# Performance work log

Hardware: AMD Instinct MI355X
Metric: run time of the kernel (lower is better)

The kernel has to match this reference:

```python
import jax, jax.numpy as jnp
import numpy as np

N = 50000      # nodes
E = 600000     # edges
D_IN = 5
D_H = 128
EPS = 1e-5     # BatchNorm1d default eps


def batch_norm(x, gamma, beta):
    # training-mode BN over the node dimension (biased variance)
    m = jnp.mean(x, axis=0)
    v = jnp.var(x, axis=0)
    return (x - m) * jax.lax.rsqrt(v + EPS) * gamma + beta


def gcn_conv(x, W, b, src, dst, w):
    # PyG GCNConv: linear transform, add self-loops (weight 1),
    # symmetric normalization D^-1/2 A D^-1/2, scatter-add to dst, + bias.
    x = x @ W                                   # [N, out]
    n = x.shape[0]
    loop = jnp.arange(n)
    src = jnp.concatenate([src, loop])
    dst = jnp.concatenate([dst, loop])
    w = jnp.concatenate([w, jnp.ones((n,), w.dtype)])
    deg = jax.ops.segment_sum(w, dst, num_segments=n)
    dis = jnp.where(deg > 0, jax.lax.rsqrt(jnp.maximum(deg, 1e-12)), 0.0)
    norm = dis[src] * w * dis[dst]              # [E+N]
    msgs = norm[:, None] * x[src]               # gather + scale
    return jax.ops.segment_sum(msgs, dst, num_segments=n) + b


def setup_inputs() -> dict:
    key = jax.random.key(0)
    ks = jax.random.split(key, 20)
    s_in = 1.0 / np.sqrt(D_IN)
    s_h = 1.0 / np.sqrt(D_H)
    return {
        "h": jax.random.normal(ks[0], (N, D_IN), jnp.float32),
        "edge_index": jax.random.randint(ks[1], (2, E), 0, N),
        "edge_weight": jax.random.uniform(ks[2], (E,), jnp.float32),
        "g0": 1.0 + 0.1 * jax.random.normal(ks[3], (D_IN,), jnp.float32),
        "be0": 0.1 * jax.random.normal(ks[4], (D_IN,), jnp.float32),
        "W1": jax.random.normal(ks[5], (D_IN, D_H), jnp.float32) * s_in,
        "b1": jax.random.normal(ks[6], (D_H,), jnp.float32) * s_in,
        "g1": 1.0 + 0.1 * jax.random.normal(ks[7], (D_H,), jnp.float32),
        "be1": 0.1 * jax.random.normal(ks[8], (D_H,), jnp.float32),
        "W2": jax.random.normal(ks[9], (D_H, D_H), jnp.float32) * s_h,
        "b2": jax.random.normal(ks[10], (D_H,), jnp.float32) * s_h,
        "g2": 1.0 + 0.1 * jax.random.normal(ks[11], (D_H,), jnp.float32),
        "be2": 0.1 * jax.random.normal(ks[12], (D_H,), jnp.float32),
        "Wmu": jax.random.normal(ks[13], (D_H, D_H), jnp.float32) * s_h,
        "bmu": jax.random.normal(ks[14], (D_H,), jnp.float32) * s_h,
        "Wls": jax.random.normal(ks[15], (D_H, D_H), jnp.float32) * s_h,
        "bls": jax.random.normal(ks[16], (D_H,), jnp.float32) * s_h,
    }


def reference(h, edge_index, edge_weight, g0, be0, W1, b1, g1, be1,
              W2, b2, g2, be2, Wmu, bmu, Wls, bls):
    src, dst = edge_index[0], edge_index[1]
    h = batch_norm(h, g0, be0)
    h = jax.nn.relu(batch_norm(gcn_conv(h, W1, b1, src, dst, edge_weight), g1, be1))
    # dropout p=0.1 treated as eval-mode (identity)
    h = jax.nn.relu(batch_norm(gcn_conv(h, W2, b2, src, dst, edge_weight), g2, be2))
    mu = h @ Wmu + bmu
    log_std = h @ Wls + bls
    return (mu, log_std)
```

## Files before the change

kernel.cpp:

```cpp
#include <hip/hip_runtime.h>

#define N_NODES 50000
#define N_EDGES 600000
#define D_IN 5
#define D_H 128
#define BN_EPS 1e-5f
#define SCAN_BLOCKS ((N_NODES + 255) / 256)
#define DEG_BLOCKS ((N_EDGES + 255) / 256)
#define FIX_SCALE 16777216.0f
#define FIX_INV   (1.0f / 16777216.0f)

typedef __bf16 bf16x8 __attribute__((ext_vector_type(8)));
typedef float  f32x4  __attribute__((ext_vector_type(4)));

__device__ inline unsigned short f2bfb(float f) {
    unsigned u = __builtin_bit_cast(unsigned, f);
    unsigned r = u + 0x7fffu + ((u >> 16) & 1u);
    return (unsigned short)(r >> 16);
}
__device__ inline float bflo(unsigned u) { return __builtin_bit_cast(float, u << 16); }
__device__ inline float bfhi(unsigned u) { return __builtin_bit_cast(float, u & 0xffff0000u); }

__device__ inline void stage_b(const unsigned short* __restrict__ Bt,
                               uint4* __restrict__ lds, int t)
{
#pragma unroll
    for (int i = 0; i < 8; ++i) {
        int slot = i * 256 + t;
        int fid = slot >> 6;
        int l = slot & 63;
        int row = (fid >> 2) * 16 + (l & 15);
        int boff = ((l >> 4) * 16 + (fid & 3) * 64) >> 1;
        lds[slot] = *(const uint4*)(Bt + row * D_H + boff);
    }
}

__global__ __launch_bounds__(256) void k_prep(const float* __restrict__ W2,
                                              const float* __restrict__ Wmu,
                                              const float* __restrict__ Wls,
                                              unsigned short* __restrict__ T2,
                                              unsigned short* __restrict__ Tmu,
                                              unsigned short* __restrict__ Tls,
                                              const float* __restrict__ h,
                                              float* __restrict__ stats0,
                                              const int* __restrict__ dst,
                                              const float* __restrict__ w,
                                              unsigned long long* __restrict__ degcnt,
                                              int* __restrict__ rank)
{
    __shared__ float ss[D_IN], sq[D_IN];
    int b = blockIdx.x;
    int t = threadIdx.x;
    if (b < 192) {
        int mat = b >> 6;
        int idx = (b & 63) * 256 + t;
        const float* W = (mat == 0) ? W2 : (mat == 1) ? Wmu : Wls;
        unsigned short* T = (mat == 0) ? T2 : (mat == 1) ? Tmu : Tls;
        int k = idx >> 7, n = idx & 127;
        T[n * D_H + k] = f2bfb(W[idx]);
    } else if (b < 192 + SCAN_BLOCKS) {
        if (t < D_IN) { ss[t] = 0.f; sq[t] = 0.f; }
        __syncthreads();
        int node = (b - 192) * 256 + t;
        float v[D_IN];
#pragma unroll
        for (int f = 0; f < D_IN; ++f)
            v[f] = (node < N_NODES) ? h[node * D_IN + f] : 0.f;
        int lane = t & 63;
#pragma unroll
        for (int f = 0; f < D_IN; ++f) {
            float s = v[f], q = v[f] * v[f];
            for (int off = 32; off > 0; off >>= 1) {
                s += __shfl_down(s, off);
                q += __shfl_down(q, off);
            }
            if (lane == 0) { atomicAdd(&ss[f], s); atomicAdd(&sq[f], q); }
        }
        __syncthreads();
        if (t < D_IN) {
            atomicAdd(&stats0[t], ss[t]);
            atomicAdd(&stats0[D_IN + t], sq[t]);
        }
    } else {
        int e = (b - 192 - SCAN_BLOCKS) * 256 + t;
        if (e < N_EDGES) {
            int d = dst[e];
            unsigned long long fx = (unsigned long long)(w[e] * FIX_SCALE + 0.5f);
            unsigned long long old = atomicAdd(degcnt + d, (1ull << 40) | fx);
            rank[e] = (int)(old >> 40);
        }
    }
}

__global__ __launch_bounds__(256) void k_scan1(const unsigned long long* __restrict__ degcnt,
                                               float* __restrict__ dis,
                                               int* __restrict__ blocksums)
{
    __shared__ int sm[256];
    int t = threadIdx.x;
    int i = blockIdx.x * 256 + t;
    int c = 0;
    if (i < N_NODES) {
        unsigned long long v = degcnt[i];
        c = (int)(v >> 40);
        float deg = (float)(v & ((1ull << 40) - 1)) * FIX_INV;
        dis[i] = rsqrtf(deg + 1.0f);
    }
    sm[t] = c;
    __syncthreads();
    for (int off = 128; off > 0; off >>= 1) {
        if (t < off) sm[t] += sm[t + off];
        __syncthreads();
    }
    if (t == 0) blocksums[blockIdx.x] = sm[0];
}

__global__ __launch_bounds__(256) void k_scan2(int* __restrict__ blocksums,
                                               int* __restrict__ rowptr)
{
    __shared__ int sm[256];
    int t = threadIdx.x;
    int c = (t < SCAN_BLOCKS) ? blocksums[t] : 0;
    sm[t] = c;
    __syncthreads();
    for (int off = 1; off < 256; off <<= 1) {
        int v = (t >= off) ? sm[t - off] : 0;
        __syncthreads();
        sm[t] += v;
        __syncthreads();
    }
    if (t < SCAN_BLOCKS) blocksums[t] = sm[t] - c;
    if (t == 255) rowptr[N_NODES] = sm[255];
}

__global__ __launch_bounds__(256) void k_scan3(const unsigned long long* __restrict__ degcnt,
                                               int* __restrict__ rowptr,
                                               const int* __restrict__ blocksums)
{
    __shared__ int sm[256];
    int t = threadIdx.x;
    int i = blockIdx.x * 256 + t;
    int c = (i < N_NODES) ? (int)(degcnt[i] >> 40) : 0;
    sm[t] = c;
    __syncthreads();
    for (int off = 1; off < 256; off <<= 1) {
        int v = (t >= off) ? sm[t - off] : 0;
        __syncthreads();
        sm[t] += v;
        __syncthreads();
    }
    if (i < N_NODES)
        rowptr[i] = blocksums[blockIdx.x] + sm[t] - c;
}

__global__ __launch_bounds__(256) void k_fill(const int* __restrict__ src,
                                              const int* __restrict__ dst,
                                              const float* __restrict__ w,
                                              const float* __restrict__ dis,
                                              const int* __restrict__ rowptr,
                                              const int* __restrict__ rank,
                                              int2* __restrict__ csr)
{
    int e = blockIdx.x * blockDim.x + threadIdx.x;
    if (e < N_EDGES) {
        int s = src[e], d = dst[e];
        float pn = dis[s] * w[e];
        int pos = rowptr[d] + rank[e];
        int2 pk;
        pk.x = s;
        pk.y = __builtin_bit_cast(int, pn);
        csr[pos] = pk;
    }
}

__global__ __launch_bounds__(256) void k_agg0(const float* __restrict__ h,
                                              const float* __restrict__ stats,
                                              const float* __restrict__ g0,
                                              const float* __restrict__ be0,
                                              const int* __restrict__ rowptr,
                                              const int2* __restrict__ csr,
                                              const float* __restrict__ dis,
                                              float* __restrict__ agg)
{
    int n = blockIdx.x * blockDim.x + threadIdx.x;
    if (n >= N_NODES) return;
    float sc[D_IN], sh[D_IN];
#pragma unroll
    for (int f = 0; f < D_IN; ++f) {
        float m = stats[f] * (1.0f / N_NODES);
        float var = stats[D_IN + f] * (1.0f / N_NODES) - m * m;
        sc[f] = rsqrtf(var + BN_EPS) * g0[f];
        sh[f] = be0[f] - m * sc[f];
    }
    float dn = dis[n];
    float acc[D_IN];
#pragma unroll
    for (int f = 0; f < D_IN; ++f)
        acc[f] = dn * (h[n * D_IN + f] * sc[f] + sh[f]);
    int e0 = rowptr[n], e1 = rowptr[n + 1];
    for (int e = e0; e < e1; ++e) {
        int2 pk = csr[e];
        int s = pk.x;
        float pn = __builtin_bit_cast(float, pk.y);
#pragma unroll
        for (int f = 0; f < D_IN; ++f)
            acc[f] += pn * (h[s * D_IN + f] * sc[f] + sh[f]);
    }
#pragma unroll
    for (int f = 0; f < D_IN; ++f)
        agg[n * D_IN + f] = dn * acc[f];
}

__global__ __launch_bounds__(256) void k_l1(const float* __restrict__ agg,
                                            const float* __restrict__ W1,
                                            const float* __restrict__ b1,
                                            unsigned short* __restrict__ x,
                                            float* __restrict__ stats)
{
    __shared__ float sm_s[D_H], sm_q[D_H];
    int t = threadIdx.x;
    if (t < D_H) { sm_s[t] = 0.f; sm_q[t] = 0.f; }
    __syncthreads();
    int idx0 = blockIdx.x * 256 + t;
    int f0 = (idx0 & 63) * 2;
    float wa[D_IN], wb[D_IN];
#pragma unroll
    for (int k = 0; k < D_IN; ++k) {
        wa[k] = W1[k * D_H + f0];
        wb[k] = W1[k * D_H + f0 + 1];
    }
    float ba = b1[f0], bb = b1[f0 + 1];
    float s0 = 0.f, q0 = 0.f, s1 = 0.f, q1 = 0.f;
    const int stride = 512 * 256;
    for (int idx = idx0; idx < N_NODES * 64; idx += stride) {
        int n = idx >> 6;
        const float* a = agg + n * D_IN;
        float v0 = ba, v1 = bb;
#pragma unroll
        for (int k = 0; k < D_IN; ++k) { v0 += wa[k] * a[k]; v1 += wb[k] * a[k]; }
        ((unsigned*)x)[idx] = (unsigned)f2bfb(v0) | ((unsigned)f2bfb(v1) << 16);
        s0 += v0; q0 += v0 * v0; s1 += v1; q1 += v1 * v1;
    }
    atomicAdd(&sm_s[f0], s0); atomicAdd(&sm_s[f0 + 1], s1);
    atomicAdd(&sm_q[f0], q0); atomicAdd(&sm_q[f0 + 1], q1);
    __syncthreads();
    if (t < D_H) {
        atomicAdd(stats + t, sm_s[t]);
        atomicAdd(stats + D_H + t, sm_q[t]);
    }
}

__global__ __launch_bounds__(256) void k_agg128(const unsigned short* __restrict__ x,
                                                const float* __restrict__ stats,
                                                const float* __restrict__ g,
                                                const float* __restrict__ be,
                                                const int* __restrict__ rowptr,
                                                const int2* __restrict__ csr,
                                                const float* __restrict__ dis,
                                                unsigned short* __restrict__ outb)
{
    int t = threadIdx.x;
    int n = blockIdx.x * 16 + (t >> 4);
    int f0 = (t & 15) * 8;
    if (n >= N_NODES) return;
    float sc[8], sh[8];
    const float inv = 1.0f / N_NODES;
#pragma unroll
    for (int j = 0; j < 8; ++j) {
        float m = stats[f0 + j] * inv;
        float var = stats[D_H + f0 + j] * inv - m * m;
        sc[j] = rsqrtf(var + BN_EPS) * g[f0 + j];
        sh[j] = be[f0 + j] - m * sc[j];
    }
#define BNR(val, j) fmaxf((val) * sc[j] + sh[j], 0.f)
    float dn = dis[n];
    uint4 hv = *(const uint4*)(x + (size_t)n * D_H + f0);
    float a0 = dn * BNR(bflo(hv.x), 0), a1 = dn * BNR(bfhi(hv.x), 1);
    float a2 = dn * BNR(bflo(hv.y), 2), a3 = dn * BNR(bfhi(hv.y), 3);
    float a4 = dn * BNR(bflo(hv.z), 4), a5 = dn * BNR(bfhi(hv.z), 5);
    float a6 = dn * BNR(bflo(hv.w), 6), a7 = dn * BNR(bfhi(hv.w), 7);
    int e = rowptr[n], e1 = rowptr[n + 1];
    for (; e + 4 <= e1; e += 4) {
        int2 p0 = csr[e + 0], p1 = csr[e + 1], p2 = csr[e + 2], p3 = csr[e + 3];
        float w0 = __builtin_bit_cast(float, p0.y);
        float w1 = __builtin_bit_cast(float, p1.y);
        float w2 = __builtin_bit_cast(float, p2.y);
        float w3 = __builtin_bit_cast(float, p3.y);
        uint4 v0 = *(const uint4*)(x + (size_t)p0.x * D_H + f0);
        uint4 v1 = *(const uint4*)(x + (size_t)p1.x * D_H + f0);
        uint4 v2 = *(const uint4*)(x + (size_t)p2.x * D_H + f0);
        uint4 v3 = *(const uint4*)(x + (size_t)p3.x * D_H + f0);
        a0 += w0 * BNR(bflo(v0.x), 0) + w1 * BNR(bflo(v1.x), 0) + w2 * BNR(bflo(v2.x), 0) + w3 * BNR(bflo(v3.x), 0);
        a1 += w0 * BNR(bfhi(v0.x), 1) + w1 * BNR(bfhi(v1.x), 1) + w2 * BNR(bfhi(v2.x), 1) + w3 * BNR(bfhi(v3.x), 1);
        a2 += w0 * BNR(bflo(v0.y), 2) + w1 * BNR(bflo(v1.y), 2) + w2 * BNR(bflo(v2.y), 2) + w3 * BNR(bflo(v3.y), 2);
        a3 += w0 * BNR(bfhi(v0.y), 3) + w1 * BNR(bfhi(v1.y), 3) + w2 * BNR(bfhi(v2.y), 3) + w3 * BNR(bfhi(v3.y), 3);
        a4 += w0 * BNR(bflo(v0.z), 4) + w1 * BNR(bflo(v1.z), 4) + w2 * BNR(bflo(v2.z), 4) + w3 * BNR(bflo(v3.z), 4);
        a5 += w0 * BNR(bfhi(v0.z), 5) + w1 * BNR(bfhi(v1.z), 5) + w2 * BNR(bfhi(v2.z), 5) + w3 * BNR(bfhi(v3.z), 5);
        a6 += w0 * BNR(bflo(v0.w), 6) + w1 * BNR(bflo(v1.w), 6) + w2 * BNR(bflo(v2.w), 6) + w3 * BNR(bflo(v3.w), 6);
        a7 += w0 * BNR(bfhi(v0.w), 7) + w1 * BNR(bfhi(v1.w), 7) + w2 * BNR(bfhi(v2.w), 7) + w3 * BNR(bfhi(v3.w), 7);
    }
    for (; e < e1; ++e) {
        int2 pk = csr[e];
        float pn = __builtin_bit_cast(float, pk.y);
        uint4 v = *(const uint4*)(x + (size_t)pk.x * D_H + f0);
        a0 += pn * BNR(bflo(v.x), 0); a1 += pn * BNR(bfhi(v.x), 1);
        a2 += pn * BNR(bflo(v.y), 2); a3 += pn * BNR(bfhi(v.y), 3);
        a4 += pn * BNR(bflo(v.z), 4); a5 += pn * BNR(bfhi(v.z), 5);
        a6 += pn * BNR(bflo(v.w), 6); a7 += pn * BNR(bfhi(v.w), 7);
    }
#undef BNR
    uint4 o;
    o.x = (unsigned)f2bfb(dn * a0) | ((unsigned)f2bfb(dn * a1) << 16);
    o.y = (unsigned)f2bfb(dn * a2) | ((unsigned)f2bfb(dn * a3) << 16);
    o.z = (unsigned)f2bfb(dn * a4) | ((unsigned)f2bfb(dn * a5) << 16);
    o.w = (unsigned)f2bfb(dn * a6) | ((unsigned)f2bfb(dn * a7) << 16);
    *(uint4*)(outb + (size_t)n * D_H + f0) = o;
}

__global__ __launch_bounds__(256) void k_gemm_mf(const unsigned short* __restrict__ A,
                                                 const unsigned short* __restrict__ Bt,
                                                 const float* __restrict__ bias,
                                                 unsigned short* __restrict__ C,
                                                 float* __restrict__ stats)
{
    __shared__ uint4 ldsB[2048];
    __shared__ float sm_s[D_H], sm_q[D_H];
    int t = threadIdx.x;
    if (t < D_H) { sm_s[t] = 0.f; sm_q[t] = 0.f; }
    stage_b(Bt, ldsB, t);
    int wave = t >> 6, lane = t & 63;
    int m = lane & 15, quad = lane >> 4;
    int r0 = blockIdx.x * 64 + wave * 16;
    int arow = r0 + m < N_NODES ? r0 + m : N_NODES - 1;
    const bf16x8* ap = (const bf16x8*)(A + (size_t)arow * D_H + quad * 8);
    bf16x8 af[4];
#pragma unroll
    for (int ks = 0; ks < 4; ++ks) af[ks] = ap[ks * 4];
    __syncthreads();
    const bf16x8* bf = (const bf16x8*)ldsB;
    f32x4 acc[8];
#pragma unroll
    for (int ct = 0; ct < 8; ++ct) acc[ct] = (f32x4)(0.f);
#pragma unroll
    for (int ks = 0; ks < 4; ++ks) {
#pragma unroll
        for (int ct = 0; ct < 8; ++ct) {
            acc[ct] = __builtin_amdgcn_mfma_f32_16x16x32_bf16(
                af[ks], bf[(ct * 4 + ks) * 64 + lane], acc[ct], 0, 0, 0);
        }
    }
#pragma unroll
    for (int ct = 0; ct < 8; ++ct) {
        int col = ct * 16 + m;
        float bv = bias[col];
        float s = 0.f, q = 0.f;
#pragma unroll
        for (int r = 0; r < 4; ++r) {
            int rr = r0 + quad * 4 + r;
            if (rr < N_NODES) {
                float v = acc[ct][r] + bv;
                C[(size_t)rr * D_H + col] = f2bfb(v);
                s += v; q += v * v;
            }
        }
        atomicAdd(&sm_s[col], s);
        atomicAdd(&sm_q[col], q);
    }
    __syncthreads();
    if (t < D_H) {
        atomicAdd(stats + t, sm_s[t]);
        atomicAdd(stats + D_H + t, sm_q[t]);
    }
}

__global__ __launch_bounds__(256) void k_gemm_out_mf(const unsigned short* __restrict__ A,
                                                     const float* __restrict__ stats,
                                                     const float* __restrict__ g,
                                                     const float* __restrict__ be,
                                                     const unsigned short* __restrict__ Btmu,
                                                     const float* __restrict__ bmu,
                                                     const unsigned short* __restrict__ Btls,
                                                     const float* __restrict__ bls,
                                                     float* __restrict__ out)
{
    __shared__ uint4 ldsB[2048];
    int t = threadIdx.x;
    int wave = t >> 6, lane = t & 63;
    int m = lane & 15, quad = lane >> 4;
    int r0 = blockIdx.x * 64 + wave * 16;
    int arow = r0 + m < N_NODES ? r0 + m : N_NODES - 1;
    const unsigned short* arowp = A + (size_t)arow * D_H + quad * 8;
    const float inv = 1.0f / N_NODES;
    bf16x8 af[4];
#pragma unroll
    for (int ks = 0; ks < 4; ++ks) {
        uint4 av = *(const uint4*)(arowp + ks * 32);
        float vals[8] = { bflo(av.x), bfhi(av.x), bflo(av.y), bfhi(av.y),
                          bflo(av.z), bfhi(av.z), bflo(av.w), bfhi(av.w) };
        int fb = quad * 8 + ks * 32;
        unsigned short o[8];
#pragma unroll
        for (int j = 0; j < 8; ++j) {
            int f = fb + j;
            float mm = stats[f] * inv;
            float var = stats[D_H + f] * inv - mm * mm;
            float scv = rsqrtf(var + BN_EPS) * g[f];
            float shv = be[f] - mm * scv;
            o[j] = f2bfb(fmaxf(vals[j] * scv + shv, 0.f));
        }
        uint4 pk;
        pk.x = (unsigned)o[0] | ((unsigned)o[1] << 16);
        pk.y = (unsigned)o[2] | ((unsigned)o[3] << 16);
        pk.z = (unsigned)o[4] | ((unsigned)o[5] << 16);
        pk.w = (unsigned)o[6] | ((unsigned)o[7] << 16);
        af[ks] = __builtin_bit_cast(bf16x8, pk);
    }
    const bf16x8* bf = (const bf16x8*)ldsB;
#pragma unroll
    for (int half = 0; half < 2; ++half) {
        if (half) __syncthreads();
        stage_b(half ? Btls : Btmu, ldsB, t);
        __syncthreads();
        const float* bias = half ? bls : bmu;
        float* C = out + (half ? (size_t)N_NODES * D_H : 0);
        f32x4 acc[8];
#pragma unroll
        for (int ct = 0; ct < 8; ++ct) acc[ct] = (f32x4)(0.f);
#pragma unroll
        for (int ks = 0; ks < 4; ++ks) {
#pragma unroll
            for (int ct = 0; ct < 8; ++ct) {
                acc[ct] = __builtin_amdgcn_mfma_f32_16x16x32_bf16(
                    af[ks], bf[(ct * 4 + ks) * 64 + lane], acc[ct], 0, 0, 0);
            }
        }
#pragma unroll
        for (int ct = 0; ct < 8; ++ct) {
            int col = ct * 16 + m;
            float bv = bias[col];
#pragma unroll
            for (int r = 0; r < 4; ++r) {
                int rr = r0 + quad * 4 + r;
                if (rr < N_NODES)
                    C[(size_t)rr * D_H + col] = acc[ct][r] + bv;
            }
        }
    }
}

extern "C" void kernel_launch(void* const* d_in, const int* in_sizes, int n_in,
                              void* d_out, int out_size, void* d_ws, size_t ws_size,
                              hipStream_t stream)
{
    const float* h   = (const float*)d_in[0];
    const int*   eidx = (const int*)d_in[1];
    const float* ew  = (const float*)d_in[2];
    const float* g0  = (const float*)d_in[3];
    const float* be0 = (const float*)d_in[4];
    const float* W1  = (const float*)d_in[5];
    const float* b1  = (const float*)d_in[6];
    const float* g1  = (const float*)d_in[7];
    const float* be1 = (const float*)d_in[8];
    const float* W2  = (const float*)d_in[9];
    const float* b2  = (const float*)d_in[10];
    const float* g2  = (const float*)d_in[11];
    const float* be2 = (const float*)d_in[12];
    const float* Wmu = (const float*)d_in[13];
    const float* bmu = (const float*)d_in[14];
    const float* Wls = (const float*)d_in[15];
    const float* bls = (const float*)d_in[16];
    const int* srcv = eidx;
    const int* dstv = eidx + N_EDGES;
    float* out = (float*)d_out;

    char* ws = (char*)d_ws;
    size_t off = 0;
    auto alloc = [&](size_t bytes) -> char* {
        char* p = ws + off;
        off += (bytes + 255) & ~(size_t)255;
        return p;
    };
    float* stats0  = (float*)alloc(16 * 4);
    float* stats1  = (float*)alloc(256 * 4);
    float* stats2  = (float*)alloc(256 * 4);
    unsigned long long* degcnt = (unsigned long long*)alloc(N_NODES * 8);
    size_t zero_bytes = off;
    int*   rowptr  = (int*)  alloc((N_NODES + 1) * 4);
    float* dis     = (float*)alloc(N_NODES * 4);
    int*   rank    = (int*)  alloc((size_t)N_EDGES * 4);
    int*   blocksums = (int*)alloc(256 * 4);
    int2*  csr     = (int2*) alloc((size_t)N_EDGES * 8);
    float* agg0    = (float*)alloc(N_NODES * D_IN * 4);
    unsigned short* x1h  = (unsigned short*)alloc((size_t)N_NODES * D_H * 2);
    unsigned short* aggh = (unsigned short*)alloc((size_t)N_NODES * D_H * 2);
    unsigned short* c2h  = (unsigned short*)alloc((size_t)N_NODES * D_H * 2);
    unsigned short* Wt2   = (unsigned short*)alloc(D_H * D_H * 2);
    unsigned short* Wtmu  = (unsigned short*)alloc(D_H * D_H * 2);
    unsigned short* Wtls  = (unsigned short*)alloc(D_H * D_H * 2);
    (void)ws_size; (void)in_sizes; (void)n_in; (void)out_size;

    hipMemsetAsync(d_ws, 0, zero_bytes, stream);

    k_prep<<<192 + SCAN_BLOCKS + DEG_BLOCKS, 256, 0, stream>>>(
        W2, Wmu, Wls, Wt2, Wtmu, Wtls, h, stats0, dstv, ew, degcnt, rank);
    k_scan1<<<SCAN_BLOCKS, 256, 0, stream>>>(degcnt, dis, blocksums);
    k_scan2<<<1, 256, 0, stream>>>(blocksums, rowptr);
    k_scan3<<<SCAN_BLOCKS, 256, 0, stream>>>(degcnt, rowptr, blocksums);
    k_fill<<<DEG_BLOCKS, 256, 0, stream>>>(srcv, dstv, ew, dis, rowptr, rank, csr);
    k_agg0<<<SCAN_BLOCKS, 256, 0, stream>>>(h, stats0, g0, be0, rowptr, csr, dis, agg0);
    k_l1<<<512, 256, 0, stream>>>(agg0, W1, b1, x1h, stats1);
    k_agg128<<<(N_NODES + 15) / 16, 256, 0, stream>>>(x1h, stats1, g1, be1,
                                                      rowptr, csr, dis, aggh);
    k_gemm_mf<<<(N_NODES + 63) / 64, 256, 0, stream>>>(aggh, Wt2, b2, c2h, stats2);
    k_gemm_out_mf<<<(N_NODES + 63) / 64, 256, 0, stream>>>(c2h, stats2, g2, be2,
                                                           Wtmu, bmu, Wtls, bls, out);
}
```

Before: 281.5 us.

## Recompute layer-1 linear in the aggregation kernel instead of materializing it

Layer 1's 5-to-128 linear output is no longer written to a bf16 buffer. k_l1 now only accumulates the BatchNorm statistics. The aggregation kernel recomputes each neighbour's 128-wide features from the padded 8-float aggregated input, so the gather reads 32 bytes per edge instead of 256 bytes of bf16, at the cost of extra FMAs per edge. Separately, the single-block block-sum scan kernel is folded into k_scan3, which removes one launch but makes every block redundantly rescan the block sums.

```diff
diff --git a/kernel.cpp b/kernel.cpp
--- a/kernel.cpp
+++ b/kernel.cpp
@@ -115,30 +115,25 @@
     if (t == 0) blocksums[blockIdx.x] = sm[0];
 }
 
-__global__ __launch_bounds__(256) void k_scan2(int* __restrict__ blocksums,
-                                               int* __restrict__ rowptr)
-{
-    __shared__ int sm[256];
-    int t = threadIdx.x;
-    int c = (t < SCAN_BLOCKS) ? blocksums[t] : 0;
-    sm[t] = c;
-    __syncthreads();
-    for (int off = 1; off < 256; off <<= 1) {
-        int v = (t >= off) ? sm[t - off] : 0;
-        __syncthreads();
-        sm[t] += v;
-        __syncthreads();
-    }
-    if (t < SCAN_BLOCKS) blocksums[t] = sm[t] - c;
-    if (t == 255) rowptr[N_NODES] = sm[255];
-}
-
 __global__ __launch_bounds__(256) void k_scan3(const unsigned long long* __restrict__ degcnt,
                                                int* __restrict__ rowptr,
                                                const int* __restrict__ blocksums)
 {
+    __shared__ int bs[256];
     __shared__ int sm[256];
     int t = threadIdx.x;
+    int bc = (t < SCAN_BLOCKS) ? blocksums[t] : 0;
+    bs[t] = bc;
+    __syncthreads();
+    for (int off = 1; off < 256; off <<= 1) {
+        int v = (t >= off) ? bs[t - off] : 0;
+        __syncthreads();
+        bs[t] += v;
+        __syncthreads();
+    }
+    int prefix = (blockIdx.x == 0) ? 0 : bs[blockIdx.x - 1];
+    if (blockIdx.x == SCAN_BLOCKS - 1 && t == 255)
+        rowptr[N_NODES] = bs[SCAN_BLOCKS - 1];
     int i = blockIdx.x * 256 + t;
     int c = (i < N_NODES) ? (int)(degcnt[i] >> 40) : 0;
     sm[t] = c;
@@ -150,7 +145,7 @@
         __syncthreads();
     }
     if (i < N_NODES)
-        rowptr[i] = blocksums[blockIdx.x] + sm[t] - c;
+        rowptr[i] = prefix + sm[t] - c;
 }
 
 __global__ __launch_bounds__(256) void k_fill(const int* __restrict__ src,
@@ -208,13 +203,12 @@
     }
 #pragma unroll
     for (int f = 0; f < D_IN; ++f)
-        agg[n * D_IN + f] = dn * acc[f];
+        agg[(size_t)n * 8 + f] = dn * acc[f];
 }
 
 __global__ __launch_bounds__(256) void k_l1(const float* __restrict__ agg,
                                             const float* __restrict__ W1,
                                             const float* __restrict__ b1,
-                                            unsigned short* __restrict__ x,
                                             float* __restrict__ stats)
 {
     __shared__ float sm_s[D_H], sm_q[D_H];
@@ -234,11 +228,10 @@
     const int stride = 512 * 256;
     for (int idx = idx0; idx < N_NODES * 64; idx += stride) {
         int n = idx >> 6;
-        const float* a = agg + n * D_IN;
+        const float* a = agg + (size_t)n * 8;
         float v0 = ba, v1 = bb;
 #pragma unroll
         for (int k = 0; k < D_IN; ++k) { v0 += wa[k] * a[k]; v1 += wb[k] * a[k]; }
-        ((unsigned*)x)[idx] = (unsigned)f2bfb(v0) | ((unsigned)f2bfb(v1) << 16);
         s0 += v0; q0 += v0 * v0; s1 += v1; q1 += v1 * v1;
     }
     atomicAdd(&sm_s[f0], s0); atomicAdd(&sm_s[f0 + 1], s1);
@@ -250,7 +243,9 @@
     }
 }
 
-__global__ __launch_bounds__(256) void k_agg128(const unsigned short* __restrict__ x,
+__global__ __launch_bounds__(256) void k_agg_l1(const float* __restrict__ agg,
+                                                const float* __restrict__ W1,
+                                                const float* __restrict__ b1,
                                                 const float* __restrict__ stats,
                                                 const float* __restrict__ g,
                                                 const float* __restrict__ be,
@@ -263,57 +258,72 @@
     int n = blockIdx.x * 16 + (t >> 4);
     int f0 = (t & 15) * 8;
     if (n >= N_NODES) return;
-    float sc[8], sh[8];
+    float wl[D_IN][8];
+#pragma unroll
+    for (int k = 0; k < D_IN; ++k) {
+        float4 wlo = *(const float4*)(W1 + k * D_H + f0);
+        float4 whi = *(const float4*)(W1 + k * D_H + f0 + 4);
+        wl[k][0] = wlo.x; wl[k][1] = wlo.y; wl[k][2] = wlo.z; wl[k][3] = wlo.w;
+        wl[k][4] = whi.x; wl[k][5] = whi.y; wl[k][6] = whi.z; wl[k][7] = whi.w;
+    }
+    float bv[8], sc[8], sh[8];
     const float inv = 1.0f / N_NODES;
 #pragma unroll
     for (int j = 0; j < 8; ++j) {
+        bv[j] = b1[f0 + j];
         float m = stats[f0 + j] * inv;
         float var = stats[D_H + f0 + j] * inv - m * m;
         sc[j] = rsqrtf(var + BN_EPS) * g[f0 + j];
         sh[j] = be[f0 + j] - m * sc[j];
     }
-#define BNR(val, j) fmaxf((val) * sc[j] + sh[j], 0.f)
     float dn = dis[n];
-    uint4 hv = *(const uint4*)(x + (size_t)n * D_H + f0);
-    float a0 = dn * BNR(bflo(hv.x), 0), a1 = dn * BNR(bfhi(hv.x), 1);
-    float a2 = dn * BNR(bflo(hv.y), 2), a3 = dn * BNR(bfhi(hv.y), 3);
-    float a4 = dn * BNR(bflo(hv.z), 4), a5 = dn * BNR(bfhi(hv.z), 5);
-    float a6 = dn * BNR(bflo(hv.w), 6), a7 = dn * BNR(bfhi(hv.w), 7);
+    float acc[8];
+    {
+        float4 a03 = *(const float4*)(agg + (size_t)n * 8);
+        float a4 = agg[(size_t)n * 8 + 4];
+#pragma unroll
+        for (int j = 0; j < 8; ++j) {
+            float v = bv[j] + wl[0][j] * a03.x + wl[1][j] * a03.y
+                    + wl[2][j] * a03.z + wl[3][j] * a03.w + wl[4][j] * a4;
+            acc[j] = dn * fmaxf(v * sc[j] + sh[j], 0.f);
+        }
+    }
     int e = rowptr[n], e1 = rowptr[n + 1];
-    for (; e + 4 <= e1; e += 4) {
-        int2 p0 = csr[e + 0], p1 = csr[e + 1], p2 = csr[e + 2], p3 = csr[e + 3];
+    for (; e + 2 <= e1; e += 2) {
+        int2 p0 = csr[e], p1 = csr[e + 1];
         float w0 = __builtin_bit_cast(float, p0.y);
         float w1 = __builtin_bit_cast(float, p1.y);
-        float w2 = __builtin_bit_cast(float, p2.y);
-        float w3 = __builtin_bit_cast(float, p3.y);
-        uint4 v0 = *(const uint4*)(x + (size_t)p0.x * D_H + f0);
-        uint4 v1 = *(const uint4*)(x + (size_t)p1.x * D_H + f0);
-        uint4 v2 = *(const uint4*)(x + (size_t)p2.x * D_H + f0);
-        uint4 v3 = *(const uint4*)(x + (size_t)p3.x * D_H + f0);
-        a0 += w0 * BNR(bflo(v0.x), 0) + w1 * BNR(bflo(v1.x), 0) + w2 * BNR(bflo(v2.x), 0) + w3 * BNR(bflo(v3.x), 0);
-        a1 += w0 * BNR(bfhi(v0.x), 1) + w1 * BNR(bfhi(v1.x), 1) + w2 * BNR(bfhi(v2.x), 1) + w3 * BNR(bfhi(v3.x), 1);
-        a2 += w0 * BNR(bflo(v0.y), 2) + w1 * BNR(bflo(v1.y), 2) + w2 * BNR(bflo(v2.y), 2) + w3 * BNR(bflo(v3.y), 2);
-        a3 += w0 * BNR(bfhi(v0.y), 3) + w1 * BNR(bfhi(v1.y), 3) + w2 * BNR(bfhi(v2.y), 3) + w3 * BNR(bfhi(v3.y), 3);
-        a4 += w0 * BNR(bflo(v0.z), 4) + w1 * BNR(bflo(v1.z), 4) + w2 * BNR(bflo(v2.z), 4) + w3 * BNR(bflo(v3.z), 4);
-        a5 += w0 * BNR(bfhi(v0.z), 5) + w1 * BNR(bfhi(v1.z), 5) + w2 * BNR(bfhi(v2.z), 5) + w3 * BNR(bfhi(v3.z), 5);
-        a6 += w0 * BNR(bflo(v0.w), 6) + w1 * BNR(bflo(v1.w), 6) + w2 * BNR(bflo(v2.w), 6) + w3 * BNR(bflo(v3.w), 6);
-        a7 += w0 * BNR(bfhi(v0.w), 7) + w1 * BNR(bfhi(v1.w), 7) + w2 * BNR(bfhi(v2.w), 7) + w3 * BNR(bfhi(v3.w), 7);
+        float4 x0 = *(const float4*)(agg + (size_t)p0.x * 8);
+        float x04 = agg[(size_t)p0.x * 8 + 4];
+        float4 x1 = *(const float4*)(agg + (size_t)p1.x * 8);
+        float x14 = agg[(size_t)p1.x * 8 + 4];
+#pragma unroll
+        for (int j = 0; j < 8; ++j) {
+            float v0 = bv[j] + wl[0][j] * x0.x + wl[1][j] * x0.y
+                     + wl[2][j] * x0.z + wl[3][j] * x0.w + wl[4][j] * x04;
+            float v1 = bv[j] + wl[0][j] * x1.x + wl[1][j] * x1.y
+                     + wl[2][j] * x1.z + wl[3][j] * x1.w + wl[4][j] * x14;
+            acc[j] += w0 * fmaxf(v0 * sc[j] + sh[j], 0.f)
+                    + w1 * fmaxf(v1 * sc[j] + sh[j], 0.f);
+        }
     }
     for (; e < e1; ++e) {
         int2 pk = csr[e];
         float pn = __builtin_bit_cast(float, pk.y);
-        uint4 v = *(const uint4*)(x + (size_t)pk.x * D_H + f0);
-        a0 += pn * BNR(bflo(v.x), 0); a1 += pn * BNR(bfhi(v.x), 1);
-        a2 += pn * BNR(bflo(v.y), 2); a3 += pn * BNR(bfhi(v.y), 3);
-        a4 += pn * BNR(bflo(v.z), 4); a5 += pn * BNR(bfhi(v.z), 5);
-        a6 += pn * BNR(bflo(v.w), 6); a7 += pn * BNR(bfhi(v.w), 7);
-    }
-#undef BNR
+        float4 x0 = *(const float4*)(agg + (size_t)pk.x * 8);
+        float x04 = agg[(size_t)pk.x * 8 + 4];
+#pragma unroll
+        for (int j = 0; j < 8; ++j) {
+            float v = bv[j] + wl[0][j] * x0.x + wl[1][j] * x0.y
+                    + wl[2][j] * x0.z + wl[3][j] * x0.w + wl[4][j] * x04;
+            acc[j] += pn * fmaxf(v * sc[j] + sh[j], 0.f);
+        }
+    }
     uint4 o;
-    o.x = (unsigned)f2bfb(dn * a0) | ((unsigned)f2bfb(dn * a1) << 16);
-    o.y = (unsigned)f2bfb(dn * a2) | ((unsigned)f2bfb(dn * a3) << 16);
-    o.z = (unsigned)f2bfb(dn * a4) | ((unsigned)f2bfb(dn * a5) << 16);
-    o.w = (unsigned)f2bfb(dn * a6) | ((unsigned)f2bfb(dn * a7) << 16);
+    o.x = (unsigned)f2bfb(dn * acc[0]) | ((unsigned)f2bfb(dn * acc[1]) << 16);
+    o.y = (unsigned)f2bfb(dn * acc[2]) | ((unsigned)f2bfb(dn * acc[3]) << 16);
+    o.z = (unsigned)f2bfb(dn * acc[4]) | ((unsigned)f2bfb(dn * acc[5]) << 16);
+    o.w = (unsigned)f2bfb(dn * acc[6]) | ((unsigned)f2bfb(dn * acc[7]) << 16);
     *(uint4*)(outb + (size_t)n * D_H + f0) = o;
 }
 
@@ -352,13 +362,13 @@
 #pragma unroll
     for (int ct = 0; ct < 8; ++ct) {
         int col = ct * 16 + m;
-        float bv = bias[col];
+        float bvv = bias[col];
         float s = 0.f, q = 0.f;
 #pragma unroll
         for (int r = 0; r < 4; ++r) {
             int rr = r0 + quad * 4 + r;
             if (rr < N_NODES) {
-                float v = acc[ct][r] + bv;
+                float v = acc[ct][r] + bvv;
                 C[(size_t)rr * D_H + col] = f2bfb(v);
                 s += v; q += v * v;
             }
@@ -437,12 +447,12 @@
 #pragma unroll
         for (int ct = 0; ct < 8; ++ct) {
             int col = ct * 16 + m;
-            float bv = bias[col];
+            float bvv = bias[col];
 #pragma unroll
             for (int r = 0; r < 4; ++r) {
                 int rr = r0 + quad * 4 + r;
                 if (rr < N_NODES)
-                    C[(size_t)rr * D_H + col] = acc[ct][r] + bv;
+                    C[(size_t)rr * D_H + col] = acc[ct][r] + bvv;
             }
         }
     }
@@ -490,8 +500,7 @@
     int*   rank    = (int*)  alloc((size_t)N_EDGES * 4);
     int*   blocksums = (int*)alloc(256 * 4);
     int2*  csr     = (int2*) alloc((size_t)N_EDGES * 8);
-    float* agg0    = (float*)alloc(N_NODES * D_IN * 4);
-    unsigned short* x1h  = (unsigned short*)alloc((size_t)N_NODES * D_H * 2);
+    float* agg0    = (float*)alloc((size_t)N_NODES * 8 * 4);
     unsigned short* aggh = (unsigned short*)alloc((size_t)N_NODES * D_H * 2);
     unsigned short* c2h  = (unsigned short*)alloc((size_t)N_NODES * D_H * 2);
     unsigned short* Wt2   = (unsigned short*)alloc(D_H * D_H * 2);
@@ -504,12 +513,11 @@
     k_prep<<<192 + SCAN_BLOCKS + DEG_BLOCKS, 256, 0, stream>>>(
         W2, Wmu, Wls, Wt2, Wtmu, Wtls, h, stats0, dstv, ew, degcnt, rank);
     k_scan1<<<SCAN_BLOCKS, 256, 0, stream>>>(degcnt, dis, blocksums);
-    k_scan2<<<1, 256, 0, stream>>>(blocksums, rowptr);
     k_scan3<<<SCAN_BLOCKS, 256, 0, stream>>>(degcnt, rowptr, blocksums);
     k_fill<<<DEG_BLOCKS, 256, 0, stream>>>(srcv, dstv, ew, dis, rowptr, rank, csr);
     k_agg0<<<SCAN_BLOCKS, 256, 0, stream>>>(h, stats0, g0, be0, rowptr, csr, dis, agg0);
-    k_l1<<<512, 256, 0, stream>>>(agg0, W1, b1, x1h, stats1);
-    k_agg128<<<(N_NODES + 15) / 16, 256, 0, stream>>>(x1h, stats1, g1, be1,
+    k_l1<<<512, 256, 0, stream>>>(agg0, W1, b1, stats1);
+    k_agg_l1<<<(N_NODES + 15) / 16, 256, 0, stream>>>(agg0, W1, b1, stats1, g1, be1,
                                                       rowptr, csr, dis, aggh);
     k_gemm_mf<<<(N_NODES + 63) / 64, 256, 0, stream>>>(aggh, Wt2, b2, c2h, stats2);
     k_gemm_out_mf<<<(N_NODES + 63) / 64, 256, 0, stream>>>(c2h, stats2, g2, be2,
```

Result: slower. 301.1 us (+7.0%).

## Fuse layer-0 aggregation with first linear layer and merge scan kernels

Applied to the files above, without the earlier changes.

Folds the block-sum scan into the per-block scan kernel, with each block redundantly scanning the block sums, which removes one launch. Fuses the 5-feature aggregation with the W1 projection and BN statistics, dropping the intermediate agg0 buffer and one launch. The fused kernel runs only one node per thread over about 196 blocks, with per-thread strided row stores. BN stats are now computed from the bf16-rounded outputs by rereading them.

```diff
diff --git a/kernel.cpp b/kernel.cpp
--- a/kernel.cpp
+++ b/kernel.cpp
@@ -20,6 +20,7 @@
 }
 __device__ inline float bflo(unsigned u) { return __builtin_bit_cast(float, u << 16); }
 __device__ inline float bfhi(unsigned u) { return __builtin_bit_cast(float, u & 0xffff0000u); }
+__device__ inline float bfs(unsigned short s) { return __builtin_bit_cast(float, (unsigned)s << 16); }
 
 __device__ inline void stage_b(const unsigned short* __restrict__ Bt,
                                uint4* __restrict__ lds, int t)
@@ -115,30 +116,25 @@
     if (t == 0) blocksums[blockIdx.x] = sm[0];
 }
 
-__global__ __launch_bounds__(256) void k_scan2(int* __restrict__ blocksums,
-                                               int* __restrict__ rowptr)
-{
-    __shared__ int sm[256];
-    int t = threadIdx.x;
-    int c = (t < SCAN_BLOCKS) ? blocksums[t] : 0;
-    sm[t] = c;
-    __syncthreads();
-    for (int off = 1; off < 256; off <<= 1) {
-        int v = (t >= off) ? sm[t - off] : 0;
-        __syncthreads();
-        sm[t] += v;
-        __syncthreads();
-    }
-    if (t < SCAN_BLOCKS) blocksums[t] = sm[t] - c;
-    if (t == 255) rowptr[N_NODES] = sm[255];
-}
-
 __global__ __launch_bounds__(256) void k_scan3(const unsigned long long* __restrict__ degcnt,
                                                int* __restrict__ rowptr,
                                                const int* __restrict__ blocksums)
 {
+    __shared__ int bs[256];
     __shared__ int sm[256];
     int t = threadIdx.x;
+    int bc = (t < SCAN_BLOCKS) ? blocksums[t] : 0;
+    bs[t] = bc;
+    __syncthreads();
+    for (int off = 1; off < 256; off <<= 1) {
+        int v = (t >= off) ? bs[t - off] : 0;
+        __syncthreads();
+        bs[t] += v;
+        __syncthreads();
+    }
+    int prefix = (blockIdx.x == 0) ? 0 : bs[blockIdx.x - 1];
+    if (blockIdx.x == SCAN_BLOCKS - 1 && t == 255)
+        rowptr[N_NODES] = bs[SCAN_BLOCKS - 1];
     int i = blockIdx.x * 256 + t;
     int c = (i < N_NODES) ? (int)(degcnt[i] >> 40) : 0;
     sm[t] = c;
@@ -150,7 +146,7 @@
         __syncthreads();
     }
     if (i < N_NODES)
-        rowptr[i] = blocksums[blockIdx.x] + sm[t] - c;
+        rowptr[i] = prefix + sm[t] - c;
 }
 
 __global__ __launch_bounds__(256) void k_fill(const int* __restrict__ src,
@@ -173,80 +169,90 @@
     }
 }
 
-__global__ __launch_bounds__(256) void k_agg0(const float* __restrict__ h,
-                                              const float* __restrict__ stats,
-                                              const float* __restrict__ g0,
-                                              const float* __restrict__ be0,
-                                              const int* __restrict__ rowptr,
-                                              const int2* __restrict__ csr,
-                                              const float* __restrict__ dis,
-                                              float* __restrict__ agg)
-{
-    int n = blockIdx.x * blockDim.x + threadIdx.x;
-    if (n >= N_NODES) return;
-    float sc[D_IN], sh[D_IN];
-#pragma unroll
-    for (int f = 0; f < D_IN; ++f) {
-        float m = stats[f] * (1.0f / N_NODES);
-        float var = stats[D_IN + f] * (1.0f / N_NODES) - m * m;
-        sc[f] = rsqrtf(var + BN_EPS) * g0[f];
-        sh[f] = be0[f] - m * sc[f];
-    }
-    float dn = dis[n];
-    float acc[D_IN];
-#pragma unroll
-    for (int f = 0; f < D_IN; ++f)
-        acc[f] = dn * (h[n * D_IN + f] * sc[f] + sh[f]);
-    int e0 = rowptr[n], e1 = rowptr[n + 1];
-    for (int e = e0; e < e1; ++e) {
-        int2 pk = csr[e];
-        int s = pk.x;
-        float pn = __builtin_bit_cast(float, pk.y);
+__global__ __launch_bounds__(256) void k_agg0l1(const float* __restrict__ h,
+                                                const float* __restrict__ stats0,
+                                                const float* __restrict__ g0,
+                                                const float* __restrict__ be0,
+                                                const int* __restrict__ rowptr,
+                                                const int2* __restrict__ csr,
+                                                const float* __restrict__ dis,
+                                                const float* __restrict__ W1,
+                                                const float* __restrict__ b1,
+                                                unsigned short* __restrict__ x1h,
+                                                float* __restrict__ stats1)
+{
+    __shared__ float w1s[D_IN * D_H];
+    __shared__ float b1s[D_H];
+    __shared__ float sm_s[D_H], sm_q[D_H];
+    int t = threadIdx.x;
+    for (int i = t; i < D_IN * D_H; i += 256) w1s[i] = W1[i];
+    if (t < D_H) { b1s[t] = b1[t]; sm_s[t] = 0.f; sm_q[t] = 0.f; }
+    __syncthreads();
+
+    int n = blockIdx.x * 256 + t;
+    if (n < N_NODES) {
+        float sc[D_IN], sh[D_IN];
+#pragma unroll
+        for (int f = 0; f < D_IN; ++f) {
+            float m = stats0[f] * (1.0f / N_NODES);
+            float var = stats0[D_IN + f] * (1.0f / N_NODES) - m * m;
+            sc[f] = rsqrtf(var + BN_EPS) * g0[f];
+            sh[f] = be0[f] - m * sc[f];
+        }
+        float dn = dis[n];
+        float acc[D_IN];
 #pragma unroll
         for (int f = 0; f < D_IN; ++f)
-            acc[f] += pn * (h[s * D_IN + f] * sc[f] + sh[f]);
-    }
-#pragma unroll
-    for (int f = 0; f < D_IN; ++f)
-        agg[n * D_IN + f] = dn * acc[f];
-}
-
-__global__ __launch_bounds__(256) void k_l1(const float* __restrict__ agg,
-                                            const float* __restrict__ W1,
-                                            const float* __restrict__ b1,
-                                            unsigned short* __restrict__ x,
-                                            float* __restrict__ stats)
-{
-    __shared__ float sm_s[D_H], sm_q[D_H];
-    int t = threadIdx.x;
-    if (t < D_H) { sm_s[t] = 0.f; sm_q[t] = 0.f; }
-    __syncthreads();
-    int idx0 = blockIdx.x * 256 + t;
-    int f0 = (idx0 & 63) * 2;
-    float wa[D_IN], wb[D_IN];
-#pragma unroll
-    for (int k = 0; k < D_IN; ++k) {
-        wa[k] = W1[k * D_H + f0];
-        wb[k] = W1[k * D_H + f0 + 1];
-    }
-    float ba = b1[f0], bb = b1[f0 + 1];
-    float s0 = 0.f, q0 = 0.f, s1 = 0.f, q1 = 0.f;
-    const int stride = 512 * 256;
-    for (int idx = idx0; idx < N_NODES * 64; idx += stride) {
-        int n = idx >> 6;
-        const float* a = agg + n * D_IN;
-        float v0 = ba, v1 = bb;
-#pragma unroll
-        for (int k = 0; k < D_IN; ++k) { v0 += wa[k] * a[k]; v1 += wb[k] * a[k]; }
-        ((unsigned*)x)[idx] = (unsigned)f2bfb(v0) | ((unsigned)f2bfb(v1) << 16);
-        s0 += v0; q0 += v0 * v0; s1 += v1; q1 += v1 * v1;
-    }
-    atomicAdd(&sm_s[f0], s0); atomicAdd(&sm_s[f0 + 1], s1);
-    atomicAdd(&sm_q[f0], q0); atomicAdd(&sm_q[f0 + 1], q1);
+            acc[f] = dn * (h[n * D_IN + f] * sc[f] + sh[f]);
+        int e0 = rowptr[n], e1 = rowptr[n + 1];
+        for (int e = e0; e < e1; ++e) {
+            int2 pk = csr[e];
+            int s = pk.x;
+            float pn = __builtin_bit_cast(float, pk.y);
+#pragma unroll
+            for (int f = 0; f < D_IN; ++f)
+                acc[f] += pn * (h[s * D_IN + f] * sc[f] + sh[f]);
+        }
+#pragma unroll
+        for (int f = 0; f < D_IN; ++f)
+            acc[f] *= dn;
+        unsigned short* nbase = x1h + (size_t)n * D_H;
+#pragma unroll
+        for (int gblk = 0; gblk < 16; ++gblk) {
+            float v[8];
+#pragma unroll
+            for (int j = 0; j < 8; ++j) {
+                int f = gblk * 8 + j;
+                float vv = b1s[f];
+#pragma unroll
+                for (int k = 0; k < D_IN; ++k) vv += acc[k] * w1s[k * D_H + f];
+                v[j] = vv;
+            }
+            uint4 pk;
+            pk.x = (unsigned)f2bfb(v[0]) | ((unsigned)f2bfb(v[1]) << 16);
+            pk.y = (unsigned)f2bfb(v[2]) | ((unsigned)f2bfb(v[3]) << 16);
+            pk.z = (unsigned)f2bfb(v[4]) | ((unsigned)f2bfb(v[5]) << 16);
+            pk.w = (unsigned)f2bfb(v[6]) | ((unsigned)f2bfb(v[7]) << 16);
+            *(uint4*)(nbase + gblk * 8) = pk;
+        }
+    }
+    __syncthreads();
+    int f = t & 127;
+    int r0 = (t >> 7) * 128;
+    float s = 0.f, q = 0.f;
+    for (int r = 0; r < 128; ++r) {
+        int n2 = blockIdx.x * 256 + r0 + r;
+        if (n2 < N_NODES) {
+            float v = bfs(x1h[(size_t)n2 * D_H + f]);
+            s += v; q += v * v;
+        }
+    }
+    atomicAdd(&sm_s[f], s);
+    atomicAdd(&sm_q[f], q);
     __syncthreads();
     if (t < D_H) {
-        atomicAdd(stats + t, sm_s[t]);
-        atomicAdd(stats + D_H + t, sm_q[t]);
+        atomicAdd(stats1 + t, sm_s[t]);
+        atomicAdd(stats1 + D_H + t, sm_q[t]);
     }
 }
 
@@ -352,13 +358,13 @@
 #pragma unroll
     for (int ct = 0; ct < 8; ++ct) {
         int col = ct * 16 + m;
-        float bv = bias[col];
+        float bvv = bias[col];
         float s = 0.f, q = 0.f;
 #pragma unroll
         for (int r = 0; r < 4; ++r) {
             int rr = r0 + quad * 4 + r;
             if (rr < N_NODES) {
-                float v = acc[ct][r] + bv;
+                float v = acc[ct][r] + bvv;
                 C[(size_t)rr * D_H + col] = f2bfb(v);
                 s += v; q += v * v;
             }
@@ -437,12 +443,12 @@
 #pragma unroll
         for (int ct = 0; ct < 8; ++ct) {
             int col = ct * 16 + m;
-            float bv = bias[col];
+            float bvv = bias[col];
 #pragma unroll
             for (int r = 0; r < 4; ++r) {
                 int rr = r0 + quad * 4 + r;
                 if (rr < N_NODES)
-                    C[(size_t)rr * D_H + col] = acc[ct][r] + bv;
+                    C[(size_t)rr * D_H + col] = acc[ct][r] + bvv;
             }
         }
     }
@@ -490,7 +496,6 @@
     int*   rank    = (int*)  alloc((size_t)N_EDGES * 4);
     int*   blocksums = (int*)alloc(256 * 4);
     int2*  csr     = (int2*) alloc((size_t)N_EDGES * 8);
-    float* agg0    = (float*)alloc(N_NODES * D_IN * 4);
     unsigned short* x1h  = (unsigned short*)alloc((size_t)N_NODES * D_H * 2);
     unsigned short* aggh = (unsigned short*)alloc((size_t)N_NODES * D_H * 2);
     unsigned short* c2h  = (unsigned short*)alloc((size_t)N_NODES * D_H * 2);
@@ -504,11 +509,10 @@
     k_prep<<<192 + SCAN_BLOCKS + DEG_BLOCKS, 256, 0, stream>>>(
         W2, Wmu, Wls, Wt2, Wtmu, Wtls, h, stats0, dstv, ew, degcnt, rank);
     k_scan1<<<SCAN_BLOCKS, 256, 0, stream>>>(degcnt, dis, blocksums);
-    k_scan2<<<1, 256, 0, stream>>>(blocksums, rowptr);
     k_scan3<<<SCAN_BLOCKS, 256, 0, stream>>>(degcnt, rowptr, blocksums);
     k_fill<<<DEG_BLOCKS, 256, 0, stream>>>(srcv, dstv, ew, dis, rowptr, rank, csr);
-    k_agg0<<<SCAN_BLOCKS, 256, 0, stream>>>(h, stats0, g0, be0, rowptr, csr, dis, agg0);
-    k_l1<<<512, 256, 0, stream>>>(agg0, W1, b1, x1h, stats1);
+    k_agg0l1<<<SCAN_BLOCKS, 256, 0, stream>>>(h, stats0, g0, be0, rowptr, csr, dis,
+                                              W1, b1, x1h, stats1);
     k_agg128<<<(N_NODES + 15) / 16, 256, 0, stream>>>(x1h, stats1, g1, be1,
                                                       rowptr, csr, dis, aggh);
     k_gemm_mf<<<(N_NODES + 63) / 64, 256, 0, stream>>>(aggh, Wt2, b2, c2h, stats2);
```

Result: slower. 293.5 us (+4.3%).
